# Performance work log

Hardware: AMD Instinct MI355X
Metric: run time of the kernel (lower is better)

## Reference

```python
import jax, jax.numpy as jnp
import numpy as np

B, LT, D, N, H = 16, 512, 1024, 4096, 16
LN_EPS = 1e-5


def setup_inputs() -> dict:
    key = jax.random.key(0)
    ks = jax.random.split(key, 10)
    s = 0.02
    struct_token = jax.random.normal(ks[0], (N, D), dtype=jnp.float32)
    text_token = jax.random.normal(ks[1], (B, LT, D), dtype=jnp.float32)
    # contiguous, sorted segment ids: 256 struct tokens per batch element
    struct_batch = jnp.repeat(jnp.arange(B, dtype=jnp.int32), N // B)
    return {
        "struct_token": struct_token,
        "text_token": text_token,
        "in_proj_w": jax.random.normal(ks[2], (3 * D, D), dtype=jnp.float32) * s,
        "in_proj_b": jnp.zeros((3 * D,), jnp.float32),
        "attn_out_w": jax.random.normal(ks[3], (D, D), dtype=jnp.float32) * s,
        "attn_out_b": jnp.zeros((D,), jnp.float32),
        "ln_g": jnp.ones((D,), jnp.float32),
        "ln_b": jnp.zeros((D,), jnp.float32),
        "proj_w": jax.random.normal(ks[4], (D, D), dtype=jnp.float32) * s,
        "proj_b": jnp.zeros((D,), jnp.float32),
        "struct_batch": struct_batch,
        "L_max": N // B,
    }


def reference(struct_token, text_token, in_proj_w, in_proj_b, attn_out_w,
              attn_out_b, ln_g, ln_b, proj_w, proj_b, struct_batch, L_max):
    Bq = text_token.shape[0]
    Dm = struct_token.shape[-1]
    dh = Dm // H
    Ntok = struct_token.shape[0]

    # ---- ragged pad-pack (struct_batch is sorted/contiguous per segment) ----
    counts = jnp.bincount(struct_batch, length=Bq)                 # [B]
    starts = jnp.concatenate([jnp.zeros((1,), counts.dtype),
                              jnp.cumsum(counts)[:-1]])            # [B]
    pos = jnp.arange(Ntok) - starts[struct_batch]                  # [N] position in segment
    padded = jnp.zeros((Bq, L_max, Dm), struct_token.dtype)
    padded = padded.at[struct_batch, pos].set(struct_token)        # [B, Ls, D]

    # ---- nn.MultiheadAttention (batch_first): Q=padded, K=V=text ----
    wq, wk, wv = in_proj_w[:Dm], in_proj_w[Dm:2 * Dm], in_proj_w[2 * Dm:]
    bq, bk, bv = in_proj_b[:Dm], in_proj_b[Dm:2 * Dm], in_proj_b[2 * Dm:]
    q = (padded @ wq.T + bq).reshape(Bq, L_max, H, dh)
    k = (text_token @ wk.T + bk).reshape(Bq, -1, H, dh)
    v = (text_token @ wv.T + bv).reshape(Bq, -1, H, dh)
    scores = jnp.einsum('bqhd,bkhd->bhqk', q, k) / jnp.sqrt(jnp.float32(dh))
    attn = jax.nn.softmax(scores, axis=-1)
    ctx = jnp.einsum('bhqk,bkhd->bqhd', attn, v).reshape(Bq, L_max, Dm)
    fused = ctx @ attn_out_w.T + attn_out_b                        # [B, Ls, D]

    # ---- LayerNorm + output projection ----
    mu = fused.mean(-1, keepdims=True)
    var = fused.var(-1, keepdims=True)
    fused = (fused - mu) * jax.lax.rsqrt(var + LN_EPS) * ln_g + ln_b
    fused = fused @ proj_w.T + proj_b

    # ---- unpack valid tokens + scatter-mean over segments ----
    tok = fused[struct_batch, pos]                                 # [N, D]
    seg_sum = jax.ops.segment_sum(tok, struct_batch, num_segments=Bq)
    return seg_sum / jnp.maximum(counts, 1)[:, None].astype(seg_sum.dtype)
```

## Files before the change

kernel.cpp:

```cpp
#include <hip/hip_runtime.h>

constexpr int B  = 16;
constexpr int LT = 512;
constexpr int D  = 1024;
constexpr int N  = 4096;
constexpr int H  = 16;
constexpr int DH = D / H;
constexpr int LMAX = N / B;
constexpr float LN_EPS = 1e-5f;

typedef short  s16x8 __attribute__((ext_vector_type(8)));
typedef float  f32x4 __attribute__((ext_vector_type(4)));

__device__ __forceinline__ unsigned short f2bf(float x) {
    unsigned int u = __float_as_uint(x);
    unsigned int r = (u + 0x7fffu + ((u >> 16) & 1u)) >> 16;
    return (unsigned short)r;
}
__device__ __forceinline__ float bf2f(unsigned short u) {
    return __uint_as_float((unsigned int)u << 16);
}

__device__ __forceinline__ void load_lds16(const void* g, void* l) {
    __builtin_amdgcn_global_load_lds(
        (const __attribute__((address_space(1))) unsigned int*)g,
        (__attribute__((address_space(3))) unsigned int*)l, 16, 0, 0);
}

__global__ __launch_bounds__(256) void cast3_prep(
        const float* __restrict__ x0, unsigned short* __restrict__ y0, int n0,
        const float* __restrict__ x1, unsigned short* __restrict__ y1, int n1,
        const float* __restrict__ x2, unsigned short* __restrict__ y2, int n2,
        const int* __restrict__ sb, int* __restrict__ counts, int* __restrict__ starts) {
    __shared__ int s_counts[B];
    int t = threadIdx.x;
    if (blockIdx.x == 6144) {
        if (t < B) s_counts[t] = 0;
        __syncthreads();
        for (int i = t; i < N; i += 256) atomicAdd(&s_counts[sb[i]], 1);
        __syncthreads();
        if (t == 0) {
            int run = 0;
            for (int b = 0; b < B; b++) { starts[b] = run; run += s_counts[b]; }
        }
        if (t < B) counts[t] = s_counts[t];
        return;
    }
    long long i = (long long)(blockIdx.x * 256 + t) * 8;
    const float* x; unsigned short* y;
    if (i < n0)                { x = x0 + i; y = y0 + i; }
    else if (i < (long long)n0 + n1) { long long j = i - n0; x = x1 + j; y = y1 + j; }
    else if (i < (long long)n0 + n1 + n2) { long long j = i - n0 - n1; x = x2 + j; y = y2 + j; }
    else return;
    float4 a = *(const float4*)x;
    float4 b = *(const float4*)(x + 4);
    ushort4 o1, o2;
    o1.x = f2bf(a.x); o1.y = f2bf(a.y); o1.z = f2bf(a.z); o1.w = f2bf(a.w);
    o2.x = f2bf(b.x); o2.y = f2bf(b.y); o2.z = f2bf(b.z); o2.w = f2bf(b.w);
    *(ushort4*)y = o1;
    *(ushort4*)(y + 4) = o2;
}

__global__ void scatter_full(const float* __restrict__ st,
                             const int* __restrict__ counts,
                             const int* __restrict__ starts,
                             unsigned short* __restrict__ padded) {
    int p = blockIdx.x, b = blockIdx.y;
    int d = threadIdx.x * 4;
    size_t off = ((size_t)(b * LMAX + p)) * D + d;
    ushort4 o = {0, 0, 0, 0};
    if (p < counts[b]) {
        float4 v = *(const float4*)&st[(size_t)(starts[b] + p) * D + d];
        o.x = f2bf(v.x); o.y = f2bf(v.y); o.z = f2bf(v.z); o.w = f2bf(v.w);
    }
    *(ushort4*)&padded[off] = o;
}

template<typename Epi>
__device__ __forceinline__ void gemm32(const unsigned short* __restrict__ A,
                                       const unsigned short* __restrict__ W,
                                       int K, int kbeg, int kend, int m0, int n0,
                                       unsigned short* __restrict__ As,
                                       unsigned short* __restrict__ Bs,
                                       Epi&& epi) {
    const int tid  = threadIdx.x;
    const int lane = tid & 63;
    const int wid  = tid >> 6;
    const int wr   = wid >> 1;
    const int wc   = wid & 1;
    const int fm   = lane & 15;
    const int quad = lane >> 4;
    const int NK   = (kend - kbeg) >> 5;

    f32x4 acc[4][4];
#pragma unroll
    for (int i = 0; i < 4; i++)
#pragma unroll
        for (int j = 0; j < 4; j++) acc[i][j] = (f32x4){0.f, 0.f, 0.f, 0.f};

    const int rA0 = tid >> 2,          sA0 = (tid & 3) ^ ((tid >> 3) & 3);
    const int cA1 = tid + 512;
    const int rA1 = cA1 >> 2,          sA1 = (cA1 & 3) ^ ((cA1 >> 3) & 3);
    const unsigned short* gA0 = A + (size_t)(m0 + rA0) * K + kbeg + sA0 * 8;
    const unsigned short* gA1 = A + (size_t)(m0 + rA1) * K + kbeg + sA1 * 8;
    const unsigned short* gB  = W + (size_t)(n0 + rA0) * K + kbeg + sA0 * 8;
    unsigned short* lA0 = As + (size_t)tid * 8;
    unsigned short* lA1 = As + (size_t)(tid + 512) * 8;
    unsigned short* lB  = Bs + (size_t)tid * 8;

    const int sl8 = (quad ^ ((fm >> 1) & 3)) * 8;
    int offA[4], offB[4];
#pragma unroll
    for (int i = 0; i < 4; i++) offA[i] = (wr * 64 + i * 16 + fm) * 32 + sl8;
#pragma unroll
    for (int j = 0; j < 4; j++) offB[j] = (wc * 64 + j * 16 + fm) * 32 + sl8;

    load_lds16(gA0, lA0);
    load_lds16(gA1, lA1);
    load_lds16(gB , lB );

    for (int s = 0; s < NK; s++) {
        const int ab = (s & 1) << 13;
        const int bb = (s & 1) << 12;
        asm volatile("s_barrier" ::: "memory");
        if (s + 1 < NK) {
            const int go = (s + 1) << 5;
            const int ab2 = ((s + 1) & 1) << 13;
            const int bb2 = ((s + 1) & 1) << 12;
            load_lds16(gA0 + go, lA0 + ab2);
            load_lds16(gA1 + go, lA1 + ab2);
            load_lds16(gB  + go, lB  + bb2);
            asm volatile("s_waitcnt vmcnt(3)" ::: "memory");
        } else {
            asm volatile("s_waitcnt vmcnt(0)" ::: "memory");
        }
        asm volatile("s_barrier" ::: "memory");

        s16x8 af[4], bfv[4];
#pragma unroll
        for (int i = 0; i < 4; i++) af[i] = *(const s16x8*)&As[ab + offA[i]];
#pragma unroll
        for (int j = 0; j < 4; j++) bfv[j] = *(const s16x8*)&Bs[bb + offB[j]];

        __builtin_amdgcn_s_setprio(1);
#pragma unroll
        for (int i = 0; i < 4; i++)
#pragma unroll
            for (int j = 0; j < 4; j++)
                acc[i][j] = __builtin_amdgcn_mfma_f32_16x16x32_bf16(af[i], bfv[j], acc[i][j], 0, 0, 0);
        __builtin_amdgcn_s_setprio(0);
    }

    const int fr = quad * 4;
#pragma unroll
    for (int i = 0; i < 4; i++)
#pragma unroll
        for (int j = 0; j < 4; j++) {
            int row = m0 + wr * 64 + i * 16 + fr;
            int col = n0 + wc * 64 + j * 16 + fm;
#pragma unroll
            for (int r = 0; r < 4; r++)
                epi(row + r, col, acc[i][j][r]);
        }
}

__global__ __launch_bounds__(512, 4) void qkv_fused(const unsigned short* __restrict__ padded,
                                                    const unsigned short* __restrict__ text,
                                                    const unsigned short* __restrict__ wqkv,
                                                    const float* __restrict__ bqkv,
                                                    unsigned short* __restrict__ qpack,
                                                    unsigned short* __restrict__ kpack,
                                                    unsigned short* __restrict__ vpack) {
    __shared__ __align__(16) unsigned short As[2 * 8192];
    __shared__ __align__(16) unsigned short Bs[2 * 4096];
    int orig = blockIdx.x;
    int id = (orig & 7) * 80 + (orig >> 3);
    if (id < 128) {
        int mt = id >> 3, nt = id & 7;
        gemm32(padded, wqkv, D, 0, D, mt * 256, nt * 128, As, Bs,
            [&](int mm, int col, float v) {
                float val = v + bqkv[col];
                int b = mm >> 8, q = mm & 255;
                int h = col >> 6, d = col & 63;
                qpack[(size_t)(b * H + h) * 16384 + (d >> 3) * 2048 + q * 8 + (d & 7)] = f2bf(val);
            });
    } else if (id < 384) {
        int f = id - 128;
        int mt = f >> 3, nt = f & 7;
        gemm32(text, wqkv + (size_t)D * D, D, 0, D, mt * 256, nt * 128, As, Bs,
            [&](int mm, int col, float v) {
                float val = v + bqkv[D + col];
                int b = mm >> 9, key = mm & 511;
                int h = col >> 6, d = col & 63;
                kpack[(size_t)(b * H + h) * 32768 + (d >> 3) * 4096 + key * 8 + (d & 7)] = f2bf(val);
            });
    } else {
        int f = id - 384;
        int mt = f >> 6, nt = f & 63;
        gemm32(wqkv + 2 * (size_t)D * D, text, D, 0, D, mt * 256, nt * 128, As, Bs,
            [&](int mm, int col, float v) {
                float val = v + bqkv[2 * D + mm];
                int h = mm >> 6, d = mm & 63;
                int b = col >> 9, key = col & 511;
                vpack[(size_t)(b * H + h) * 32768 + (key >> 3) * 512 + d * 8 + (key & 7)] = f2bf(val);
            });
    }
}

__global__ __launch_bounds__(512, 4) void gemm_bf2(const unsigned short* __restrict__ A,
                                                   const unsigned short* __restrict__ W,
                                                   unsigned short* __restrict__ C0,
                                                   unsigned short* __restrict__ C1,
                                                   int Nn, int K) {
    __shared__ __align__(16) unsigned short As[2 * 8192];
    __shared__ __align__(16) unsigned short Bs[2 * 4096];
    int orig = blockIdx.x;
    int id = (orig & 7) * 32 + (orig >> 3);
    int kh = id >> 7;
    int f  = id & 127;
    int mt = f >> 3, nt = f & 7;
    unsigned short* C = kh ? C1 : C0;
    gemm32(A, W, K, kh * 512, (kh + 1) * 512, mt * 256, nt * 128, As, Bs,
        [&](int mm, int col, float v) {
            C[(size_t)mm * Nn + col] = f2bf(v);
        });
}

constexpr int PKW = 72;

__global__ __launch_bounds__(512) void attn_mfma(const unsigned short* __restrict__ qpack,
                                                 const unsigned short* __restrict__ kpack,
                                                 const unsigned short* __restrict__ vpack,
                                                 unsigned short* __restrict__ ctx) {
    __shared__ __align__(16) unsigned short KV[2][16384];
    __shared__ __align__(16) unsigned short Ps[8 * 16 * PKW];

    const int tid = threadIdx.x;
    const int lane = tid & 63;
    const int wv = tid >> 6;
    const int fm = lane & 15;
    const int quad = lane >> 4;
    const int h = blockIdx.x, b = blockIdx.y, half = blockIdx.z;
    const int q0 = half * 128 + wv * 16;

    const unsigned short* qp = qpack + (size_t)(b * H + h) * 16384;
    const unsigned short* kp = kpack + (size_t)(b * H + h) * 32768;
    const unsigned short* vp = vpack + (size_t)(b * H + h) * 32768;

    const s16x8 aq0 = *(const s16x8*)&qp[quad * 2048 + (q0 + fm) * 8];
    const s16x8 aq1 = *(const s16x8*)&qp[(4 + quad) * 2048 + (q0 + fm) * 8];

#pragma unroll
    for (int kc = 0; kc < 2; kc++)
#pragma unroll
        for (int it = 0; it < 4; it++) {
            int f = it * 512 + tid;
            load_lds16(kp + (f >> 8) * 4096 + kc * 2048 + (f & 255) * 8, &KV[kc][f * 8]);
        }

    f32x4 sc[32];

    asm volatile("s_waitcnt vmcnt(4)" ::: "memory");
    __builtin_amdgcn_s_barrier();
    __builtin_amdgcn_s_setprio(1);
#pragma unroll
    for (int t = 0; t < 16; t++) {
        s16x8 bk0 = *(const s16x8*)&KV[0][quad * 2048 + (t * 16 + fm) * 8];
        s16x8 bk1 = *(const s16x8*)&KV[0][(4 + quad) * 2048 + (t * 16 + fm) * 8];
        f32x4 a = (f32x4){0.f, 0.f, 0.f, 0.f};
        a = __builtin_amdgcn_mfma_f32_16x16x32_bf16(aq0, bk0, a, 0, 0, 0);
        a = __builtin_amdgcn_mfma_f32_16x16x32_bf16(aq1, bk1, a, 0, 0, 0);
        sc[t] = a;
    }
    __builtin_amdgcn_s_setprio(0);

    asm volatile("s_waitcnt vmcnt(0)" ::: "memory");
    __builtin_amdgcn_s_barrier();
    __builtin_amdgcn_s_setprio(1);
#pragma unroll
    for (int t = 0; t < 16; t++) {
        s16x8 bk0 = *(const s16x8*)&KV[1][quad * 2048 + (t * 16 + fm) * 8];
        s16x8 bk1 = *(const s16x8*)&KV[1][(4 + quad) * 2048 + (t * 16 + fm) * 8];
        f32x4 a = (f32x4){0.f, 0.f, 0.f, 0.f};
        a = __builtin_amdgcn_mfma_f32_16x16x32_bf16(aq0, bk0, a, 0, 0, 0);
        a = __builtin_amdgcn_mfma_f32_16x16x32_bf16(aq1, bk1, a, 0, 0, 0);
        sc[16 + t] = a;
    }
    __builtin_amdgcn_s_setprio(0);

    asm volatile("s_waitcnt lgkmcnt(0)" ::: "memory");
    __builtin_amdgcn_s_barrier();

#pragma unroll
    for (int vc = 0; vc < 2; vc++)
#pragma unroll
        for (int it = 0; it < 4; it++) {
            int f = it * 512 + tid;
            load_lds16(vp + vc * 16384 + f * 8, &KV[vc][f * 8]);
        }

    const float scale = 0.125f;
    float mx[4], l[4], inv[4];
#pragma unroll
    for (int r = 0; r < 4; r++) {
        float m = sc[0][r];
#pragma unroll
        for (int t = 1; t < 32; t++) m = fmaxf(m, sc[t][r]);
        mx[r] = m;
    }
#pragma unroll
    for (int o = 1; o < 16; o <<= 1)
#pragma unroll
        for (int r = 0; r < 4; r++) mx[r] = fmaxf(mx[r], __shfl_xor(mx[r], o));
#pragma unroll
    for (int r = 0; r < 4; r++) l[r] = 0.f;
#pragma unroll
    for (int t = 0; t < 32; t++)
#pragma unroll
        for (int r = 0; r < 4; r++) {
            float e = __expf((sc[t][r] - mx[r]) * scale);
            sc[t][r] = e;
            l[r] += e;
        }
#pragma unroll
    for (int o = 1; o < 16; o <<= 1)
#pragma unroll
        for (int r = 0; r < 4; r++) l[r] += __shfl_xor(l[r], o);
#pragma unroll
    for (int r = 0; r < 4; r++) inv[r] = 1.f / l[r];

    f32x4 co[4];
#pragma unroll
    for (int n = 0; n < 4; n++) co[n] = (f32x4){0.f, 0.f, 0.f, 0.f};
    unsigned short* Pw = Ps + wv * (16 * PKW);

    asm volatile("s_waitcnt vmcnt(4)" ::: "memory");
    __builtin_amdgcn_s_barrier();

    for (int vc = 0; vc < 2; vc++) {
        if (vc == 1) {
            asm volatile("s_waitcnt vmcnt(0)" ::: "memory");
            __builtin_amdgcn_s_barrier();
        }
        for (int cs = 0; cs < 4; cs++) {
            int c = vc * 4 + cs;
#pragma unroll
            for (int tt = 0; tt < 4; tt++)
#pragma unroll
                for (int r = 0; r < 4; r++)
                    Pw[(quad * 4 + r) * PKW + tt * 16 + fm] = f2bf(sc[c * 4 + tt][r]);
            __builtin_amdgcn_s_setprio(1);
#pragma unroll
            for (int s = 0; s < 2; s++) {
                s16x8 ap = *(const s16x8*)&Pw[fm * PKW + s * 32 + quad * 8];
#pragma unroll
                for (int n = 0; n < 4; n++) {
                    s16x8 bv = *(const s16x8*)&KV[vc][(cs * 8 + s * 4 + quad) * 512 + (n * 16 + fm) * 8];
                    co[n] = __builtin_amdgcn_mfma_f32_16x16x32_bf16(ap, bv, co[n], 0, 0, 0);
                }
            }
            __builtin_amdgcn_s_setprio(0);
        }
    }

    const size_t obase = (size_t)(b * LMAX + q0) * D + h * DH;
#pragma unroll
    for (int n = 0; n < 4; n++)
#pragma unroll
        for (int r = 0; r < 4; r++)
            ctx[obase + (size_t)(quad * 4 + r) * D + n * 16 + fm] = f2bf(co[n][r] * inv[r]);
}

__global__ __launch_bounds__(256) void lnmean_kernel(const unsigned short* __restrict__ f1a,
                                                     const unsigned short* __restrict__ f1b,
                                                     const float* __restrict__ bo,
                                                     const float* __restrict__ g,
                                                     const float* __restrict__ bb,
                                                     const int* __restrict__ counts,
                                                     float* __restrict__ msum) {
    int b = blockIdx.x;
    int t = threadIdx.x;
    int wv = t >> 6, lane = t & 63;
    int cnt = counts[b];
    int s0 = blockIdx.y * 32 + wv * 8;
    int s1 = min(cnt, s0 + 8);

    float4 gg[4], bv[4], bo4[4];
#pragma unroll
    for (int c = 0; c < 4; c++) {
        gg[c]  = *(const float4*)&g[c * 256 + lane * 4];
        bv[c]  = *(const float4*)&bb[c * 256 + lane * 4];
        bo4[c] = *(const float4*)&bo[c * 256 + lane * 4];
    }
    float4 acc[4];
#pragma unroll
    for (int c = 0; c < 4; c++) acc[c] = (float4){0.f, 0.f, 0.f, 0.f};

    for (int s = s0; s < s1; s++) {
        size_t rbase = ((size_t)(b * LMAX + s)) * D;
        float4 v[4];
        float sm = 0.f, ss = 0.f;
#pragma unroll
        for (int c = 0; c < 4; c++) {
            ushort4 ua = *(const ushort4*)&f1a[rbase + c * 256 + lane * 4];
            ushort4 ub = *(const ushort4*)&f1b[rbase + c * 256 + lane * 4];
            v[c].x = bf2f(ua.x) + bf2f(ub.x) + bo4[c].x;
            v[c].y = bf2f(ua.y) + bf2f(ub.y) + bo4[c].y;
            v[c].z = bf2f(ua.z) + bf2f(ub.z) + bo4[c].z;
            v[c].w = bf2f(ua.w) + bf2f(ub.w) + bo4[c].w;
            sm += v[c].x + v[c].y + v[c].z + v[c].w;
            ss += v[c].x * v[c].x + v[c].y * v[c].y + v[c].z * v[c].z + v[c].w * v[c].w;
        }
#pragma unroll
        for (int o = 32; o; o >>= 1) { sm += __shfl_xor(sm, o); ss += __shfl_xor(ss, o); }
        float mu = sm * (1.f / D);
        float var = ss * (1.f / D) - mu * mu;
        float r = rsqrtf(var + LN_EPS);
#pragma unroll
        for (int c = 0; c < 4; c++) {
            acc[c].x += (v[c].x - mu) * r * gg[c].x + bv[c].x;
            acc[c].y += (v[c].y - mu) * r * gg[c].y + bv[c].y;
            acc[c].z += (v[c].z - mu) * r * gg[c].z + bv[c].z;
            acc[c].w += (v[c].w - mu) * r * gg[c].w + bv[c].w;
        }
    }
    float inv = 1.f / (float)max(cnt, 1);
#pragma unroll
    for (int c = 0; c < 4; c++) {
        int base = b * D + c * 256 + lane * 4;
        atomicAdd(&msum[base + 0], acc[c].x * inv);
        atomicAdd(&msum[base + 1], acc[c].y * inv);
        atomicAdd(&msum[base + 2], acc[c].z * inv);
        atomicAdd(&msum[base + 3], acc[c].w * inv);
    }
}

__global__ __launch_bounds__(256) void tproj_kernel(const float* __restrict__ msum,
                                                    const float* __restrict__ W,
                                                    const float* __restrict__ bias,
                                                    float* __restrict__ out) {
    int lane = threadIdx.x & 63;
    int n = blockIdx.x * 4 + (threadIdx.x >> 6);
    float4 wr[4];
#pragma unroll
    for (int i = 0; i < 4; i++)
        wr[i] = *(const float4*)&W[(size_t)n * D + i * 256 + lane * 4];
    float bn = bias[n];
    for (int b = 0; b < B; b++) {
        float s = 0.f;
#pragma unroll
        for (int i = 0; i < 4; i++) {
            float4 m4 = *(const float4*)&msum[(size_t)b * D + i * 256 + lane * 4];
            s += m4.x * wr[i].x + m4.y * wr[i].y + m4.z * wr[i].z + m4.w * wr[i].w;
        }
#pragma unroll
        for (int o = 32; o; o >>= 1) s += __shfl_xor(s, o);
        if (lane == 0) out[(size_t)b * D + n] = s + bn;
    }
}

extern "C" void kernel_launch(void* const* d_in, const int* in_sizes, int n_in,
                              void* d_out, int out_size, void* d_ws, size_t ws_size,
                              hipStream_t stream) {
    const float* struct_token = (const float*)d_in[0];
    const float* text_token   = (const float*)d_in[1];
    const float* in_proj_w    = (const float*)d_in[2];
    const float* in_proj_b    = (const float*)d_in[3];
    const float* attn_out_w   = (const float*)d_in[4];
    const float* attn_out_b   = (const float*)d_in[5];
    const float* ln_g         = (const float*)d_in[6];
    const float* ln_b         = (const float*)d_in[7];
    const float* proj_w       = (const float*)d_in[8];
    const float* proj_b       = (const float*)d_in[9];
    const int*   sb           = (const int*)d_in[10];
    float* out = (float*)d_out;

    const size_t MQ  = (size_t)B * LMAX;
    const size_t MKV = (size_t)B * LT;

    char* p = (char*)d_ws;
    unsigned short* padded_b = (unsigned short*)p;  p += MQ * D * 2;
    unsigned short* text_b   = (unsigned short*)p;  p += MKV * D * 2;
    unsigned short* wqkv_b   = (unsigned short*)p;  p += (size_t)3 * D * D * 2;
    unsigned short* wattn_b  = (unsigned short*)p;  p += (size_t)D * D * 2;
    unsigned short* qpack    = (unsigned short*)p;  p += MQ * D * 2;
    unsigned short* kpack    = (unsigned short*)p;  p += MKV * D * 2;
    unsigned short* vpack    = (unsigned short*)p;  p += MKV * D * 2;
    unsigned short* ctx_b    = (unsigned short*)p;  p += MQ * D * 2;
    unsigned short* f1a      = (unsigned short*)p;  p += MQ * D * 2;
    unsigned short* f1b      = (unsigned short*)p;  p += MQ * D * 2;
    float* msum = (float*)p;  p += (size_t)B * D * 4;
    int* counts = (int*)p;  p += B * 4;
    int* starts = (int*)p;  p += B * 4;

    hipMemsetAsync(msum, 0, (size_t)B * D * 4, stream);

    cast3_prep<<<6145, 256, 0, stream>>>(
        text_token, text_b, (int)(MKV * D),
        in_proj_w,  wqkv_b, 3 * D * D,
        attn_out_w, wattn_b, D * D,
        sb, counts, starts);

    scatter_full<<<dim3(LMAX, B), 256, 0, stream>>>(struct_token, counts, starts, padded_b);

    qkv_fused<<<640, 512, 0, stream>>>(padded_b, text_b, wqkv_b, in_proj_b,
                                       qpack, kpack, vpack);

    attn_mfma<<<dim3(H, B, 2), 512, 0, stream>>>(qpack, kpack, vpack, ctx_b);

    gemm_bf2<<<256, 512, 0, stream>>>(ctx_b, wattn_b, f1a, f1b, D, D);

    lnmean_kernel<<<dim3(B, 8), 256, 0, stream>>>(f1a, f1b, attn_out_b, ln_g, ln_b, counts, msum);

    tproj_kernel<<<256, 256, 0, stream>>>(msum, proj_w, proj_b, out);
}
```

Before: 259.0 us.

## Fold msum zeroing into prep kernel, use 128x128 tiles for out-proj GEMM, widen LN grid

Removes the separate hipMemsetAsync by having an extra block of the cast/prep kernel zero the mean accumulator. The attention output-projection GEMM moves from 256x128 tiles with 512 threads to a new 128x128 tile path with 256 threads, doubling the block count to 512 for better CU coverage. The LayerNorm-mean kernel grid is doubled so each wave handles 4 rows instead of 8. The aim is more parallelism on small launches and one fewer launch, at the cost of less reuse per GEMM tile and more atomic contention on msum.

```diff
diff --git a/kernel.cpp b/kernel.cpp
--- a/kernel.cpp
+++ b/kernel.cpp
@@ -31,7 +31,8 @@
         const float* __restrict__ x0, unsigned short* __restrict__ y0, int n0,
         const float* __restrict__ x1, unsigned short* __restrict__ y1, int n1,
         const float* __restrict__ x2, unsigned short* __restrict__ y2, int n2,
-        const int* __restrict__ sb, int* __restrict__ counts, int* __restrict__ starts) {
+        const int* __restrict__ sb, int* __restrict__ counts, int* __restrict__ starts,
+        float* __restrict__ msum) {
     __shared__ int s_counts[B];
     int t = threadIdx.x;
     if (blockIdx.x == 6144) {
@@ -44,6 +45,13 @@
             for (int b = 0; b < B; b++) { starts[b] = run; run += s_counts[b]; }
         }
         if (t < B) counts[t] = s_counts[t];
+        return;
+    }
+    if (blockIdx.x == 6145) {
+        float4 z = {0.f, 0.f, 0.f, 0.f};
+#pragma unroll
+        for (int c = 0; c < 16; c++)
+            ((float4*)msum)[c * 256 + t] = z;
         return;
     }
     long long i = (long long)(blockIdx.x * 256 + t) * 8;
@@ -131,6 +139,95 @@
             load_lds16(gA1 + go, lA1 + ab2);
             load_lds16(gB  + go, lB  + bb2);
             asm volatile("s_waitcnt vmcnt(3)" ::: "memory");
+        } else {
+            asm volatile("s_waitcnt vmcnt(0)" ::: "memory");
+        }
+        asm volatile("s_barrier" ::: "memory");
+
+        s16x8 af[4], bfv[4];
+#pragma unroll
+        for (int i = 0; i < 4; i++) af[i] = *(const s16x8*)&As[ab + offA[i]];
+#pragma unroll
+        for (int j = 0; j < 4; j++) bfv[j] = *(const s16x8*)&Bs[bb + offB[j]];
+
+        __builtin_amdgcn_s_setprio(1);
+#pragma unroll
+        for (int i = 0; i < 4; i++)
+#pragma unroll
+            for (int j = 0; j < 4; j++)
+                acc[i][j] = __builtin_amdgcn_mfma_f32_16x16x32_bf16(af[i], bfv[j], acc[i][j], 0, 0, 0);
+        __builtin_amdgcn_s_setprio(0);
+    }
+
+    const int fr = quad * 4;
+#pragma unroll
+    for (int i = 0; i < 4; i++)
+#pragma unroll
+        for (int j = 0; j < 4; j++) {
+            int row = m0 + wr * 64 + i * 16 + fr;
+            int col = n0 + wc * 64 + j * 16 + fm;
+#pragma unroll
+            for (int r = 0; r < 4; r++)
+                epi(row + r, col, acc[i][j][r]);
+        }
+}
+
+template<typename Epi>
+__device__ __forceinline__ void gemm128(const unsigned short* __restrict__ A,
+                                        const unsigned short* __restrict__ W,
+                                        int K, int kbeg, int kend, int m0, int n0,
+                                        unsigned short* __restrict__ As,
+                                        unsigned short* __restrict__ Bs,
+                                        Epi&& epi) {
+    const int tid  = threadIdx.x;
+    const int lane = tid & 63;
+    const int wid  = tid >> 6;
+    const int wr   = wid >> 1;
+    const int wc   = wid & 1;
+    const int fm   = lane & 15;
+    const int quad = lane >> 4;
+    const int NK   = (kend - kbeg) >> 5;
+
+    f32x4 acc[4][4];
+#pragma unroll
+    for (int i = 0; i < 4; i++)
+#pragma unroll
+        for (int j = 0; j < 4; j++) acc[i][j] = (f32x4){0.f, 0.f, 0.f, 0.f};
+
+    const int r0 = tid >> 2, s0 = (tid & 3) ^ ((tid >> 3) & 3);
+    const unsigned short* gA0 = A + (size_t)(m0 + r0) * K + kbeg + s0 * 8;
+    const unsigned short* gA1 = gA0 + (size_t)64 * K;
+    const unsigned short* gB0 = W + (size_t)(n0 + r0) * K + kbeg + s0 * 8;
+    const unsigned short* gB1 = gB0 + (size_t)64 * K;
+    unsigned short* lA0 = As + (size_t)tid * 8;
+    unsigned short* lA1 = As + (size_t)(tid + 256) * 8;
+    unsigned short* lB0 = Bs + (size_t)tid * 8;
+    unsigned short* lB1 = Bs + (size_t)(tid + 256) * 8;
+
+    const int sl8 = (quad ^ ((fm >> 1) & 3)) * 8;
+    int offA[4], offB[4];
+#pragma unroll
+    for (int i = 0; i < 4; i++) offA[i] = (wr * 64 + i * 16 + fm) * 32 + sl8;
+#pragma unroll
+    for (int j = 0; j < 4; j++) offB[j] = (wc * 64 + j * 16 + fm) * 32 + sl8;
+
+    load_lds16(gA0, lA0);
+    load_lds16(gA1, lA1);
+    load_lds16(gB0, lB0);
+    load_lds16(gB1, lB1);
+
+    for (int s = 0; s < NK; s++) {
+        const int ab = (s & 1) << 12;
+        const int bb = (s & 1) << 12;
+        asm volatile("s_barrier" ::: "memory");
+        if (s + 1 < NK) {
+            const int go = (s + 1) << 5;
+            const int nb = ((s + 1) & 1) << 12;
+            load_lds16(gA0 + go, lA0 + nb);
+            load_lds16(gA1 + go, lA1 + nb);
+            load_lds16(gB0 + go, lB0 + nb);
+            load_lds16(gB1 + go, lB1 + nb);
+            asm volatile("s_waitcnt vmcnt(4)" ::: "memory");
         } else {
             asm volatile("s_waitcnt vmcnt(0)" ::: "memory");
         }
@@ -207,20 +304,20 @@
     }
 }
 
-__global__ __launch_bounds__(512, 4) void gemm_bf2(const unsigned short* __restrict__ A,
+__global__ __launch_bounds__(256, 4) void gemm_bf2(const unsigned short* __restrict__ A,
                                                    const unsigned short* __restrict__ W,
                                                    unsigned short* __restrict__ C0,
                                                    unsigned short* __restrict__ C1,
                                                    int Nn, int K) {
-    __shared__ __align__(16) unsigned short As[2 * 8192];
+    __shared__ __align__(16) unsigned short As[2 * 4096];
     __shared__ __align__(16) unsigned short Bs[2 * 4096];
     int orig = blockIdx.x;
-    int id = (orig & 7) * 32 + (orig >> 3);
-    int kh = id >> 7;
-    int f  = id & 127;
+    int id = (orig & 7) * 64 + (orig >> 3);
+    int kh = id >> 8;
+    int f  = id & 255;
     int mt = f >> 3, nt = f & 7;
     unsigned short* C = kh ? C1 : C0;
-    gemm32(A, W, K, kh * 512, (kh + 1) * 512, mt * 256, nt * 128, As, Bs,
+    gemm128(A, W, K, kh * 512, (kh + 1) * 512, mt * 128, nt * 128, As, Bs,
         [&](int mm, int col, float v) {
             C[(size_t)mm * Nn + col] = f2bf(v);
         });
@@ -382,8 +479,8 @@
     int t = threadIdx.x;
     int wv = t >> 6, lane = t & 63;
     int cnt = counts[b];
-    int s0 = blockIdx.y * 32 + wv * 8;
-    int s1 = min(cnt, s0 + 8);
+    int s0 = blockIdx.y * 16 + wv * 4;
+    int s1 = min(cnt, s0 + 4);
 
     float4 gg[4], bv[4], bo4[4];
 #pragma unroll
@@ -493,13 +590,11 @@
     int* counts = (int*)p;  p += B * 4;
     int* starts = (int*)p;  p += B * 4;
 
-    hipMemsetAsync(msum, 0, (size_t)B * D * 4, stream);
-
-    cast3_prep<<<6145, 256, 0, stream>>>(
+    cast3_prep<<<6146, 256, 0, stream>>>(
         text_token, text_b, (int)(MKV * D),
         in_proj_w,  wqkv_b, 3 * D * D,
         attn_out_w, wattn_b, D * D,
-        sb, counts, starts);
+        sb, counts, starts, msum);
 
     scatter_full<<<dim3(LMAX, B), 256, 0, stream>>>(struct_token, counts, starts, padded_b);
 
@@ -508,9 +603,9 @@
 
     attn_mfma<<<dim3(H, B, 2), 512, 0, stream>>>(qpack, kpack, vpack, ctx_b);
 
-    gemm_bf2<<<256, 512, 0, stream>>>(ctx_b, wattn_b, f1a, f1b, D, D);
-
-    lnmean_kernel<<<dim3(B, 8), 256, 0, stream>>>(f1a, f1b, attn_out_b, ln_g, ln_b, counts, msum);
+    gemm_bf2<<<512, 256, 0, stream>>>(ctx_b, wattn_b, f1a, f1b, D, D);
+
+    lnmean_kernel<<<dim3(B, 16), 256, 0, stream>>>(f1a, f1b, attn_out_b, ln_g, ln_b, counts, msum);
 
     tproj_kernel<<<256, 256, 0, stream>>>(msum, proj_w, proj_b, out);
 }
```

Result: slower. 264.3 us (+2.1%).

## Shrink GEMM tiles to 128x128 with 256-thread blocks and fold memset into prep

Applied to the files above, without the earlier changes.

The shared bf16 GEMM core drops from 256x128 tiles with 8 waves to 128x128 tiles with 4 waves. The QKV and output-projection launches double their block counts, and the block-index remapping is updated to match. This should raise the number of blocks and occupancy across the CUs and halve LDS per block, at the cost of less operand reuse per tile. The separate hipMemsetAsync of the mean accumulator is replaced by an extra block in the cast/prep kernel, removing one launch.

```diff
diff --git a/kernel.cpp b/kernel.cpp
--- a/kernel.cpp
+++ b/kernel.cpp
@@ -31,7 +31,8 @@
         const float* __restrict__ x0, unsigned short* __restrict__ y0, int n0,
         const float* __restrict__ x1, unsigned short* __restrict__ y1, int n1,
         const float* __restrict__ x2, unsigned short* __restrict__ y2, int n2,
-        const int* __restrict__ sb, int* __restrict__ counts, int* __restrict__ starts) {
+        const int* __restrict__ sb, int* __restrict__ counts, int* __restrict__ starts,
+        float* __restrict__ msum) {
     __shared__ int s_counts[B];
     int t = threadIdx.x;
     if (blockIdx.x == 6144) {
@@ -44,6 +45,13 @@
             for (int b = 0; b < B; b++) { starts[b] = run; run += s_counts[b]; }
         }
         if (t < B) counts[t] = s_counts[t];
+        return;
+    }
+    if (blockIdx.x == 6145) {
+        float4 z = {0.f, 0.f, 0.f, 0.f};
+#pragma unroll
+        for (int c = 0; c < 16; c++)
+            ((float4*)msum)[c * 256 + t] = z;
         return;
     }
     long long i = (long long)(blockIdx.x * 256 + t) * 8;
@@ -77,12 +85,12 @@
 }
 
 template<typename Epi>
-__device__ __forceinline__ void gemm32(const unsigned short* __restrict__ A,
-                                       const unsigned short* __restrict__ W,
-                                       int K, int kbeg, int kend, int m0, int n0,
-                                       unsigned short* __restrict__ As,
-                                       unsigned short* __restrict__ Bs,
-                                       Epi&& epi) {
+__device__ __forceinline__ void gemm128(const unsigned short* __restrict__ A,
+                                        const unsigned short* __restrict__ W,
+                                        int K, int kbeg, int kend, int m0, int n0,
+                                        unsigned short* __restrict__ As,
+                                        unsigned short* __restrict__ Bs,
+                                        Epi&& epi) {
     const int tid  = threadIdx.x;
     const int lane = tid & 63;
     const int wid  = tid >> 6;
@@ -98,15 +106,15 @@
 #pragma unroll
         for (int j = 0; j < 4; j++) acc[i][j] = (f32x4){0.f, 0.f, 0.f, 0.f};
 
-    const int rA0 = tid >> 2,          sA0 = (tid & 3) ^ ((tid >> 3) & 3);
-    const int cA1 = tid + 512;
-    const int rA1 = cA1 >> 2,          sA1 = (cA1 & 3) ^ ((cA1 >> 3) & 3);
-    const unsigned short* gA0 = A + (size_t)(m0 + rA0) * K + kbeg + sA0 * 8;
-    const unsigned short* gA1 = A + (size_t)(m0 + rA1) * K + kbeg + sA1 * 8;
-    const unsigned short* gB  = W + (size_t)(n0 + rA0) * K + kbeg + sA0 * 8;
+    const int r0 = tid >> 2, s0 = (tid & 3) ^ ((tid >> 3) & 3);
+    const unsigned short* gA0 = A + (size_t)(m0 + r0) * K + kbeg + s0 * 8;
+    const unsigned short* gA1 = gA0 + (size_t)64 * K;
+    const unsigned short* gB0 = W + (size_t)(n0 + r0) * K + kbeg + s0 * 8;
+    const unsigned short* gB1 = gB0 + (size_t)64 * K;
     unsigned short* lA0 = As + (size_t)tid * 8;
-    unsigned short* lA1 = As + (size_t)(tid + 512) * 8;
-    unsigned short* lB  = Bs + (size_t)tid * 8;
+    unsigned short* lA1 = As + (size_t)(tid + 256) * 8;
+    unsigned short* lB0 = Bs + (size_t)tid * 8;
+    unsigned short* lB1 = Bs + (size_t)(tid + 256) * 8;
 
     const int sl8 = (quad ^ ((fm >> 1) & 3)) * 8;
     int offA[4], offB[4];
@@ -117,20 +125,21 @@
 
     load_lds16(gA0, lA0);
     load_lds16(gA1, lA1);
-    load_lds16(gB , lB );
+    load_lds16(gB0, lB0);
+    load_lds16(gB1, lB1);
 
     for (int s = 0; s < NK; s++) {
-        const int ab = (s & 1) << 13;
+        const int ab = (s & 1) << 12;
         const int bb = (s & 1) << 12;
         asm volatile("s_barrier" ::: "memory");
         if (s + 1 < NK) {
             const int go = (s + 1) << 5;
-            const int ab2 = ((s + 1) & 1) << 13;
-            const int bb2 = ((s + 1) & 1) << 12;
-            load_lds16(gA0 + go, lA0 + ab2);
-            load_lds16(gA1 + go, lA1 + ab2);
-            load_lds16(gB  + go, lB  + bb2);
-            asm volatile("s_waitcnt vmcnt(3)" ::: "memory");
+            const int nb = ((s + 1) & 1) << 12;
+            load_lds16(gA0 + go, lA0 + nb);
+            load_lds16(gA1 + go, lA1 + nb);
+            load_lds16(gB0 + go, lB0 + nb);
+            load_lds16(gB1 + go, lB1 + nb);
+            asm volatile("s_waitcnt vmcnt(4)" ::: "memory");
         } else {
             asm volatile("s_waitcnt vmcnt(0)" ::: "memory");
         }
@@ -164,30 +173,30 @@
         }
 }
 
-__global__ __launch_bounds__(512, 4) void qkv_fused(const unsigned short* __restrict__ padded,
+__global__ __launch_bounds__(256, 4) void qkv_fused(const unsigned short* __restrict__ padded,
                                                     const unsigned short* __restrict__ text,
                                                     const unsigned short* __restrict__ wqkv,
                                                     const float* __restrict__ bqkv,
                                                     unsigned short* __restrict__ qpack,
                                                     unsigned short* __restrict__ kpack,
                                                     unsigned short* __restrict__ vpack) {
-    __shared__ __align__(16) unsigned short As[2 * 8192];
+    __shared__ __align__(16) unsigned short As[2 * 4096];
     __shared__ __align__(16) unsigned short Bs[2 * 4096];
     int orig = blockIdx.x;
-    int id = (orig & 7) * 80 + (orig >> 3);
-    if (id < 128) {
+    int id = (orig & 7) * 160 + (orig >> 3);
+    if (id < 256) {
         int mt = id >> 3, nt = id & 7;
-        gemm32(padded, wqkv, D, 0, D, mt * 256, nt * 128, As, Bs,
+        gemm128(padded, wqkv, D, 0, D, mt * 128, nt * 128, As, Bs,
             [&](int mm, int col, float v) {
                 float val = v + bqkv[col];
                 int b = mm >> 8, q = mm & 255;
                 int h = col >> 6, d = col & 63;
                 qpack[(size_t)(b * H + h) * 16384 + (d >> 3) * 2048 + q * 8 + (d & 7)] = f2bf(val);
             });
-    } else if (id < 384) {
-        int f = id - 128;
+    } else if (id < 768) {
+        int f = id - 256;
         int mt = f >> 3, nt = f & 7;
-        gemm32(text, wqkv + (size_t)D * D, D, 0, D, mt * 256, nt * 128, As, Bs,
+        gemm128(text, wqkv + (size_t)D * D, D, 0, D, mt * 128, nt * 128, As, Bs,
             [&](int mm, int col, float v) {
                 float val = v + bqkv[D + col];
                 int b = mm >> 9, key = mm & 511;
@@ -195,9 +204,9 @@
                 kpack[(size_t)(b * H + h) * 32768 + (d >> 3) * 4096 + key * 8 + (d & 7)] = f2bf(val);
             });
     } else {
-        int f = id - 384;
+        int f = id - 768;
         int mt = f >> 6, nt = f & 63;
-        gemm32(wqkv + 2 * (size_t)D * D, text, D, 0, D, mt * 256, nt * 128, As, Bs,
+        gemm128(wqkv + 2 * (size_t)D * D, text, D, 0, D, mt * 128, nt * 128, As, Bs,
             [&](int mm, int col, float v) {
                 float val = v + bqkv[2 * D + mm];
                 int h = mm >> 6, d = mm & 63;
@@ -207,20 +216,20 @@
     }
 }
 
-__global__ __launch_bounds__(512, 4) void gemm_bf2(const unsigned short* __restrict__ A,
+__global__ __launch_bounds__(256, 4) void gemm_bf2(const unsigned short* __restrict__ A,
                                                    const unsigned short* __restrict__ W,
                                                    unsigned short* __restrict__ C0,
                                                    unsigned short* __restrict__ C1,
                                                    int Nn, int K) {
-    __shared__ __align__(16) unsigned short As[2 * 8192];
+    __shared__ __align__(16) unsigned short As[2 * 4096];
     __shared__ __align__(16) unsigned short Bs[2 * 4096];
     int orig = blockIdx.x;
-    int id = (orig & 7) * 32 + (orig >> 3);
-    int kh = id >> 7;
-    int f  = id & 127;
+    int id = (orig & 7) * 64 + (orig >> 3);
+    int kh = id >> 8;
+    int f  = id & 255;
     int mt = f >> 3, nt = f & 7;
     unsigned short* C = kh ? C1 : C0;
-    gemm32(A, W, K, kh * 512, (kh + 1) * 512, mt * 256, nt * 128, As, Bs,
+    gemm128(A, W, K, kh * 512, (kh + 1) * 512, mt * 128, nt * 128, As, Bs,
         [&](int mm, int col, float v) {
             C[(size_t)mm * Nn + col] = f2bf(v);
         });
@@ -493,22 +502,20 @@
     int* counts = (int*)p;  p += B * 4;
     int* starts = (int*)p;  p += B * 4;
 
-    hipMemsetAsync(msum, 0, (size_t)B * D * 4, stream);
-
-    cast3_prep<<<6145, 256, 0, stream>>>(
+    cast3_prep<<<6146, 256, 0, stream>>>(
         text_token, text_b, (int)(MKV * D),
         in_proj_w,  wqkv_b, 3 * D * D,
         attn_out_w, wattn_b, D * D,
-        sb, counts, starts);
+        sb, counts, starts, msum);
 
     scatter_full<<<dim3(LMAX, B), 256, 0, stream>>>(struct_token, counts, starts, padded_b);
 
-    qkv_fused<<<640, 512, 0, stream>>>(padded_b, text_b, wqkv_b, in_proj_b,
-                                       qpack, kpack, vpack);
+    qkv_fused<<<1280, 256, 0, stream>>>(padded_b, text_b, wqkv_b, in_proj_b,
+                                        qpack, kpack, vpack);
 
     attn_mfma<<<dim3(H, B, 2), 512, 0, stream>>>(qpack, kpack, vpack, ctx_b);
 
-    gemm_bf2<<<256, 512, 0, stream>>>(ctx_b, wattn_b, f1a, f1b, D, D);
+    gemm_bf2<<<512, 256, 0, stream>>>(ctx_b, wattn_b, f1a, f1b, D, D);
 
     lnmean_kernel<<<dim3(B, 8), 256, 0, stream>>>(f1a, f1b, attn_out_b, ln_g, ln_b, counts, msum);
 
```

Result: faster. 248.1 us, median of 3 (-4.2%).
